# Performance work log

Measured on AMD Instinct MI355X. Metric: run time of the kernel, lower is better.

The kernel has to match this reference:

```python
import jax, jax.numpy as jnp
import numpy as np

# Gemma-style paged attention, decode-heavy continuous batching
B = 16            # number of sequences in the batch
BLOCK = 64        # KV-cache block size (tokens per block)
MAX_BLOCKS = 32   # max blocks per sequence -> max 2048 KV tokens
NUM_BLOCKS = B * MAX_BLOCKS  # 512 total cache blocks
MAX_KV = MAX_BLOCKS * BLOCK  # 2048
HQ, HK, D = 16, 8, 256       # query heads, kv heads (GQA), head_dim
HIDDEN = 3072
MAX_Q = 4                    # max new (query) tokens per sequence
ROPE_BASE = 10000.0


def setup_inputs() -> dict:
    key = jax.random.key(0)
    ks = jax.random.split(key, 7)
    # deterministic ragged layout
    q_seqlens = np.array([1 + (i % 4) for i in range(B)], np.int64)        # sum = 40
    kv_seqlens = np.array([1024 + (i * 67) % 1025 for i in range(B)], np.int64)
    q_start_loc = np.concatenate([[0], np.cumsum(q_seqlens)[:-1]]).astype(np.int64)
    T = int(q_seqlens.sum())
    history = kv_seqlens - q_seqlens
    position_ids_1d = np.concatenate(
        [np.arange(history[i], kv_seqlens[i]) for i in range(B)]).astype(np.int64)
    block_offsets = np.arange(NUM_BLOCKS, dtype=np.int64).reshape(B, MAX_BLOCKS)
    inv_freq = (1.0 / ROPE_BASE ** (np.arange(0, D, 2) / D)).astype(np.float32)
    return {
        'hidden_states': jax.random.normal(ks[0], (T, HIDDEN), jnp.float32),
        'Wq': jax.random.normal(ks[1], (HIDDEN, HQ * D), jnp.float32) * 0.02,
        'Wk': jax.random.normal(ks[2], (HIDDEN, HK * D), jnp.float32) * 0.02,
        'Wv': jax.random.normal(ks[3], (HIDDEN, HK * D), jnp.float32) * 0.02,
        'Wo': jax.random.normal(ks[4], (HQ * D, HIDDEN), jnp.float32) * 0.02,
        'k_cache': jax.random.normal(ks[5], (NUM_BLOCKS, BLOCK, HK, D), jnp.float32),
        'v_cache': jax.random.normal(ks[6], (NUM_BLOCKS, BLOCK, HK, D), jnp.float32),
        'inv_freq': jnp.asarray(inv_freq),
        'position_ids_1d': jnp.asarray(position_ids_1d),
        'q_start_loc': jnp.asarray(q_start_loc),
        'q_seqlens': jnp.asarray(q_seqlens),
        'kv_seqlens': jnp.asarray(kv_seqlens),
        'block_offsets': jnp.asarray(block_offsets),
    }


def reference(hidden_states, Wq, Wk, Wv, Wo, k_cache, v_cache, inv_freq,
              position_ids_1d, q_start_loc, q_seqlens, kv_seqlens, block_offsets):
    T = hidden_states.shape[0]
    # fused QKV projection
    q = (hidden_states @ Wq).reshape(T, HQ, D)
    k = (hidden_states @ Wk).reshape(T, HK, D)
    v = (hidden_states @ Wv).reshape(T, HK, D)
    # fused rotary embedding (neox / rotate-half style, per-token position ids)
    freqs = position_ids_1d.astype(jnp.float32)[:, None] * inv_freq[None, :]  # [T, D/2]
    cos = jnp.cos(freqs)[:, None, :]
    sin = jnp.sin(freqs)[:, None, :]

    def rope(x):
        x1, x2 = jnp.split(x, 2, axis=-1)
        return jnp.concatenate([x1 * cos - x2 * sin, x2 * cos + x1 * sin], axis=-1)

    q = rope(q)
    k = rope(k)
    # ---- fill_kv_cache: scatter new K/V into paged block cache ----
    tok = jnp.arange(T)
    seq_end = jnp.cumsum(q_seqlens)
    seq_id = jnp.searchsorted(seq_end, tok, side='right')      # sequence of each token
    off = tok - q_start_loc[seq_id]                             # offset within new tokens
    kv_pos = (kv_seqlens - q_seqlens)[seq_id] + off             # absolute kv position
    blk = block_offsets[seq_id, kv_pos // BLOCK]
    slot = kv_pos % BLOCK
    k_cache = k_cache.at[blk, slot].set(k)
    v_cache = v_cache.at[blk, slot].set(v)
    # ---- paged_attention_fwd ----
    # gather each sequence's blocks -> [B, MAX_KV, HK, D]
    k_seq = k_cache[block_offsets].reshape(B, MAX_KV, HK, D)
    v_seq = v_cache[block_offsets].reshape(B, MAX_KV, HK, D)
    # pad queries per sequence -> [B, MAX_Q, HK, G, D]
    qidx = jnp.clip(q_start_loc[:, None] + jnp.arange(MAX_Q)[None, :], 0, T - 1)
    G = HQ // HK
    qpad = q[qidx].reshape(B, MAX_Q, HK, G, D)
    scale = jnp.float32(D) ** -0.5
    scores = jnp.einsum('bqkgd,bskd->bkgqs', qpad * scale, k_seq)  # [B,HK,G,MAX_Q,MAX_KV]
    # causal mask over absolute kv positions (also masks padded kv slots)
    jpos = jnp.arange(MAX_Q)[None, :, None]
    spos = jnp.arange(MAX_KV)[None, None, :]
    mask = spos <= ((kv_seqlens - q_seqlens)[:, None, None] + jpos)  # [B,MAX_Q,MAX_KV]
    scores = jnp.where(mask[:, None, None, :, :], scores, jnp.float32(-1e30))
    attn = jax.nn.softmax(scores, axis=-1)
    out = jnp.einsum('bkgqs,bskd->bqkgd', attn, v_seq).reshape(B, MAX_Q, HQ * D)
    # scatter padded output back to flat token layout
    out_flat = out[seq_id, off]  # [T, HQ*D]
    return out_flat @ Wo
```

## Files before the change

kernel.cpp:

```cpp
#include <hip/hip_runtime.h>
#include <math.h>

#define TT 40
#define NB 16
#define HQn 16
#define HKn 8
#define Gn 2
#define Dn 256
#define HID 3072
#define QKV_COLS 8192
#define NCHUNK 16
#define CHUNKT 128

__global__ __launch_bounds__(256) void k1_qkv_gemm(
    const float* __restrict__ hs, const float* __restrict__ Wq,
    const float* __restrict__ Wk, const float* __restrict__ Wv,
    float* __restrict__ part1) {
  const int tile = blockIdx.x & 31;
  const int ks = blockIdx.x >> 5;
  const int c0 = tile << 8;
  const float* W; int ld, cw0;
  if (tile < 16)      { W = Wq; ld = 4096; cw0 = c0; }
  else if (tile < 24) { W = Wk; ld = 2048; cw0 = c0 - 4096; }
  else                { W = Wv; ld = 2048; cw0 = c0 - 6144; }
  const int kbase = ks * 192;
  const int cq = (threadIdx.x & 63) << 2;
  const int r0 = (threadIdx.x >> 6) * 10;
  __shared__ float h_lds[40][64];
  float acc[10][4];
#pragma unroll
  for (int r = 0; r < 10; ++r) { acc[r][0]=0.f; acc[r][1]=0.f; acc[r][2]=0.f; acc[r][3]=0.f; }
  for (int kc = 0; kc < 192; kc += 64) {
    __syncthreads();
    for (int i = threadIdx.x; i < 2560; i += 256) {
      int t = i >> 6, kk = i & 63;
      h_lds[t][kk] = hs[t * HID + kbase + kc + kk];
    }
    __syncthreads();
    const float* wp = W + (size_t)(kbase + kc) * ld + cw0 + cq;
#pragma unroll 8
    for (int kk = 0; kk < 64; ++kk) {
      float4 w4 = *reinterpret_cast<const float4*>(wp + (size_t)kk * ld);
#pragma unroll
      for (int r = 0; r < 10; ++r) {
        float h = h_lds[r0 + r][kk];
        acc[r][0] = fmaf(h, w4.x, acc[r][0]);
        acc[r][1] = fmaf(h, w4.y, acc[r][1]);
        acc[r][2] = fmaf(h, w4.z, acc[r][2]);
        acc[r][3] = fmaf(h, w4.w, acc[r][3]);
      }
    }
  }
#pragma unroll
  for (int r = 0; r < 10; ++r) {
    int t = r0 + r;
    float4 v = make_float4(acc[r][0], acc[r][1], acc[r][2], acc[r][3]);
    *reinterpret_cast<float4*>(&part1[(size_t)(ks * TT + t) * QKV_COLS + c0 + cq]) = v;
  }
}

__global__ __launch_bounds__(256) void k2_reduce_rope(
    const float* __restrict__ part1, const float* __restrict__ inv_freq,
    const int* __restrict__ pos_ids,
    float* __restrict__ qbuf, float* __restrict__ kbuf, float* __restrict__ vbuf) {
  const int t = blockIdx.x >> 5;
  const int tile = blockIdx.x & 31;
  const int c = (tile << 8) + threadIdx.x;
  float s = 0.f;
#pragma unroll
  for (int ks = 0; ks < 16; ++ks) s += part1[(size_t)(ks * TT + t) * QKV_COLS + c];
  __shared__ float sl[256];
  sl[threadIdx.x] = s;
  __syncthreads();
  if (tile < 24) {
    const int d = threadIdx.x;
    const int d2 = d & 127;
    float fr = (float)pos_ids[t] * inv_freq[d2];
    float cs = cosf(fr), sn = sinf(fr);
    float v = (d < 128) ? (sl[d] * cs - sl[d + 128] * sn)
                        : (sl[d] * cs + sl[d - 128] * sn);
    if (tile < 16) qbuf[t * 4096 + (tile << 8) + d] = v * 0.0625f;
    else           kbuf[t * 2048 + ((tile - 16) << 8) + d] = v;
  } else {
    vbuf[t * 2048 + ((tile - 24) << 8) + threadIdx.x] = s;
  }
}

__global__ __launch_bounds__(256) void k3_attn_partial(
    const float* __restrict__ qbuf, const float* __restrict__ kbuf,
    const float* __restrict__ vbuf, const float* __restrict__ k_cache,
    const float* __restrict__ v_cache, const int* __restrict__ blk_off,
    const int* __restrict__ q_start, const int* __restrict__ q_lens,
    const int* __restrict__ kv_lens,
    float* __restrict__ part_o, float* __restrict__ part_ml) {
  const int chunk = blockIdx.x & 15;
  const int hk = (blockIdx.x >> 4) & 7;
  const int b = blockIdx.x >> 7;
  const int kv_len = kv_lens[b];
  const int cs0 = chunk * CHUNKT;
  if (cs0 >= kv_len) return;
  const int q_cnt = q_lens[b];
  const int hist = kv_len - q_cnt;
  const int q0 = q_start[b];
  const int nq = q_cnt * 2;

  __shared__ float q_lds[8][256];
  __shared__ float S2[2][128][8];
  __shared__ float red[32][8];
  __shared__ float Mg[8];
  __shared__ float obuf[4][8][256];

  const int tid = threadIdx.x;
  const int w = tid >> 6;
  const int lane = tid & 63;
  const int tp = lane & 7;
  const int qd = lane >> 3;

  const int bi = (b << 5) + (cs0 >> 6);
  const int blk0v = blk_off[bi];
  const int blk1v = blk_off[bi + 1];
  const float* kb0  = k_cache + ((size_t)blk0v << 17) + ((size_t)hk << 8);
  const float* kb1  = k_cache + ((size_t)blk1v << 17) + ((size_t)hk << 8);
  const float* vb0  = v_cache + ((size_t)blk0v << 17) + ((size_t)hk << 8);
  const float* vb1  = v_cache + ((size_t)blk1v << 17) + ((size_t)hk << 8);
  const float* knew = kbuf + ((size_t)q0 << 11) + ((size_t)hk << 8);
  const float* vnew = vbuf + ((size_t)q0 << 11) + ((size_t)hk << 8);

  auto rowK = [&](int s) -> const float* {
    if (s < hist) {
      const float* base = (s & 64) ? kb1 : kb0;
      return base + ((size_t)(s & 63) << 11);
    }
    return knew + ((size_t)(s - hist) << 11);
  };
  auto rowV = [&](int s) -> const float* {
    if (s < hist) {
      const float* base = (s & 64) ? vb1 : vb0;
      return base + ((size_t)(s & 63) << 11);
    }
    return vnew + ((size_t)(s - hist) << 11);
  };

  for (int i = tid; i < 2048; i += 256) {
    int qv = i >> 8, d = i & 255;
    int qtok = min(qv >> 1, q_cnt - 1);
    q_lds[qv][d] = qbuf[(size_t)(q0 + qtok) * 4096 + (hk * Gn + (qv & 1)) * 256 + d];
  }
  __syncthreads();

  const int sBeg = cs0 + (w << 5);

  const float* kr[4];
#pragma unroll
  for (int tt = 0; tt < 4; ++tt) {
    int s = sBeg + (tp << 2) + tt;
    int sc = s < kv_len ? s : kv_len - 1;
    kr[tt] = rowK(sc) + (qd << 2);
  }
  float acc[4][8];
#pragma unroll
  for (int tt = 0; tt < 4; ++tt)
#pragma unroll
    for (int qv = 0; qv < 8; ++qv) acc[tt][qv] = 0.f;

#pragma unroll
  for (int c = 0; c < 8; ++c) {
    float4 kf[4];
#pragma unroll
    for (int tt = 0; tt < 4; ++tt)
      kf[tt] = *reinterpret_cast<const float4*>(kr[tt] + (c << 5));
#pragma unroll
    for (int qv = 0; qv < 8; ++qv) {
      float4 qf = *reinterpret_cast<const float4*>(&q_lds[qv][(qd << 2) + (c << 5)]);
#pragma unroll
      for (int tt = 0; tt < 4; ++tt) {
        acc[tt][qv] = fmaf(qf.x, kf[tt].x, acc[tt][qv]);
        acc[tt][qv] = fmaf(qf.y, kf[tt].y, acc[tt][qv]);
        acc[tt][qv] = fmaf(qf.z, kf[tt].z, acc[tt][qv]);
        acc[tt][qv] = fmaf(qf.w, kf[tt].w, acc[tt][qv]);
      }
    }
  }
#pragma unroll
  for (int tt = 0; tt < 4; ++tt)
#pragma unroll
    for (int qv = 0; qv < 8; ++qv) {
      float v = acc[tt][qv];
      v += __shfl_xor(v, 8);
      v += __shfl_xor(v, 16);
      acc[tt][qv] = v;
    }
  if ((lane & 24) == 0) {
    const int h = lane >> 5;
#pragma unroll
    for (int tt = 0; tt < 4; ++tt) {
      int srel = (w << 5) + (tp << 2) + tt;
      *reinterpret_cast<float4*>(&S2[h][srel][0]) =
          make_float4(acc[tt][0], acc[tt][1], acc[tt][2], acc[tt][3]);
      *reinterpret_cast<float4*>(&S2[h][srel][4]) =
          make_float4(acc[tt][4], acc[tt][5], acc[tt][6], acc[tt][7]);
    }
  }
  __syncthreads();

  const int qv2 = tid & 7;
  const int grp = tid >> 3;
  float sv[4];
  {
    float mloc = -1e30f;
#pragma unroll
    for (int t = 0; t < 4; ++t) {
      int sl = (grp << 2) + t;
      float v = S2[0][sl][qv2] + S2[1][sl][qv2];
      bool valid = (qv2 < nq) && ((cs0 + sl - hist) <= (qv2 >> 1));
      v = valid ? v : -1e30f;
      sv[t] = v;
      mloc = fmaxf(mloc, v);
    }
    red[grp][qv2] = mloc;
  }
  __syncthreads();
  if (tid < 8) {
    float M = -1e30f;
#pragma unroll
    for (int i = 0; i < 32; ++i) M = fmaxf(M, red[i][tid]);
    Mg[tid] = M;
  }
  __syncthreads();
  {
    float M = Mg[qv2];
    float lloc = 0.f;
#pragma unroll
    for (int t = 0; t < 4; ++t) {
      float p = __expf(sv[t] - M);
      S2[0][(grp << 2) + t][qv2] = p;
      lloc += p;
    }
    red[grp][qv2] = lloc;
  }
  __syncthreads();
  if (tid < 8) {
    float L = 0.f;
#pragma unroll
    for (int i = 0; i < 32; ++i) L += red[i][tid];
    int pidx = (((b * HKn + hk) * NCHUNK + chunk) << 3) + tid;
    part_ml[pidx * 2] = Mg[tid];
    part_ml[pidx * 2 + 1] = L;
  }

  float4 pacc[8];
#pragma unroll
  for (int q = 0; q < 8; ++q) pacc[q] = make_float4(0.f, 0.f, 0.f, 0.f);
  const int d4 = lane << 2;
#pragma unroll 4
  for (int t = 0; t < 32; ++t) {
    int s = sBeg + t;
    int sc = s < kv_len ? s : kv_len - 1;
    float4 vf = *reinterpret_cast<const float4*>(rowV(sc) + d4);
    int srel = (w << 5) + t;
    float4 p0 = *reinterpret_cast<const float4*>(&S2[0][srel][0]);
    float4 p1 = *reinterpret_cast<const float4*>(&S2[0][srel][4]);
    float pr[8] = {p0.x, p0.y, p0.z, p0.w, p1.x, p1.y, p1.z, p1.w};
#pragma unroll
    for (int q = 0; q < 8; ++q) {
      pacc[q].x = fmaf(pr[q], vf.x, pacc[q].x);
      pacc[q].y = fmaf(pr[q], vf.y, pacc[q].y);
      pacc[q].z = fmaf(pr[q], vf.z, pacc[q].z);
      pacc[q].w = fmaf(pr[q], vf.w, pacc[q].w);
    }
  }
#pragma unroll
  for (int q = 0; q < 8; ++q)
    *reinterpret_cast<float4*>(&obuf[w][q][d4]) = pacc[q];
  __syncthreads();

  for (int q = 0; q < nq; ++q) {
    float o = obuf[0][q][tid] + obuf[1][q][tid] + obuf[2][q][tid] + obuf[3][q][tid];
    int pidx = (((b * HKn + hk) * NCHUNK + chunk) << 3) + q;
    part_o[(size_t)pidx * 256 + tid] = o;
  }
}

__global__ __launch_bounds__(64) void k4_attn_reduce(
    const float* __restrict__ part_o, const float* __restrict__ part_ml,
    const int* __restrict__ q_start, const int* __restrict__ q_lens,
    const int* __restrict__ kv_lens, float* __restrict__ attn_out) {
  const int h = blockIdx.x & 15;
  const int qtok = (blockIdx.x >> 4) & 3;
  const int b = blockIdx.x >> 6;
  const int q_cnt = q_lens[b];
  if (qtok >= q_cnt) return;
  const int kv_len = kv_lens[b];
  const int nparts = (kv_len + CHUNKT - 1) >> 7;
  const int qv = qtok * 2 + (h & 1);
  const int hk = h >> 1;
  const int lane = threadIdx.x;
  const int pbase = ((b * HKn + hk) * NCHUNK) << 3;
  float2 mls[16];
#pragma unroll
  for (int i = 0; i < 16; ++i)
    if (i < nparts)
      mls[i] = *reinterpret_cast<const float2*>(&part_ml[(size_t)(pbase + (i << 3) + qv) * 2]);
  float M = -1e30f;
#pragma unroll
  for (int i = 0; i < 16; ++i)
    if (i < nparts) M = fmaxf(M, mls[i].x);
  float4 o = make_float4(0.f, 0.f, 0.f, 0.f);
  float L = 0.f;
#pragma unroll
  for (int i = 0; i < 16; ++i)
    if (i < nparts) {
      float corr = __expf(mls[i].x - M);
      L += corr * mls[i].y;
      float4 pv = *reinterpret_cast<const float4*>(
          &part_o[(size_t)(pbase + (i << 3) + qv) * 256 + (lane << 2)]);
      o.x = fmaf(corr, pv.x, o.x);
      o.y = fmaf(corr, pv.y, o.y);
      o.z = fmaf(corr, pv.z, o.z);
      o.w = fmaf(corr, pv.w, o.w);
    }
  float inv = 1.0f / L;
  int tr = q_start[b] + qtok;
  float4 res = make_float4(o.x * inv, o.y * inv, o.z * inv, o.w * inv);
  *reinterpret_cast<float4*>(&attn_out[((size_t)tr * HQn + h) * 256 + (lane << 2)]) = res;
}

__global__ __launch_bounds__(256) void k5_out_gemm(
    const float* __restrict__ ain, const float* __restrict__ Wo,
    float* __restrict__ part2) {
  const int tile = blockIdx.x % 12;
  const int ks = blockIdx.x / 12;
  const int c0 = tile << 8;
  const int kbase = ks << 7;
  const int cq = (threadIdx.x & 63) << 2;
  const int r0 = (threadIdx.x >> 6) * 10;
  __shared__ float h_lds[40][64];
  float acc[10][4];
#pragma unroll
  for (int r = 0; r < 10; ++r) { acc[r][0]=0.f; acc[r][1]=0.f; acc[r][2]=0.f; acc[r][3]=0.f; }
  for (int kc = 0; kc < 128; kc += 64) {
    __syncthreads();
    for (int i = threadIdx.x; i < 2560; i += 256) {
      int t = i >> 6, kk = i & 63;
      h_lds[t][kk] = ain[(size_t)t * 4096 + kbase + kc + kk];
    }
    __syncthreads();
    const float* wp = Wo + (size_t)(kbase + kc) * 3072 + c0 + cq;
#pragma unroll 8
    for (int kk = 0; kk < 64; ++kk) {
      float4 w4 = *reinterpret_cast<const float4*>(wp + (size_t)kk * 3072);
#pragma unroll
      for (int r = 0; r < 10; ++r) {
        float h = h_lds[r0 + r][kk];
        acc[r][0] = fmaf(h, w4.x, acc[r][0]);
        acc[r][1] = fmaf(h, w4.y, acc[r][1]);
        acc[r][2] = fmaf(h, w4.z, acc[r][2]);
        acc[r][3] = fmaf(h, w4.w, acc[r][3]);
      }
    }
  }
#pragma unroll
  for (int r = 0; r < 10; ++r) {
    int t = r0 + r;
    float4 v = make_float4(acc[r][0], acc[r][1], acc[r][2], acc[r][3]);
    *reinterpret_cast<float4*>(&part2[(size_t)(ks * TT + t) * 3072 + c0 + cq]) = v;
  }
}

__global__ __launch_bounds__(256) void k6_final_reduce(
    const float* __restrict__ part2, float* __restrict__ out) {
  const int idx = blockIdx.x * 256 + threadIdx.x;
  float s = 0.f;
#pragma unroll
  for (int ks = 0; ks < 32; ++ks) s += part2[(size_t)ks * 122880 + idx];
  out[idx] = s;
}

extern "C" void kernel_launch(void* const* d_in, const int* in_sizes, int n_in,
                              void* d_out, int out_size, void* d_ws, size_t ws_size,
                              hipStream_t stream) {
  const float* hs       = (const float*)d_in[0];
  const float* Wq       = (const float*)d_in[1];
  const float* Wk       = (const float*)d_in[2];
  const float* Wv       = (const float*)d_in[3];
  const float* Wo       = (const float*)d_in[4];
  const float* k_cache  = (const float*)d_in[5];
  const float* v_cache  = (const float*)d_in[6];
  const float* inv_freq = (const float*)d_in[7];
  const int*   pos_ids  = (const int*)d_in[8];
  const int*   q_start  = (const int*)d_in[9];
  const int*   q_lens   = (const int*)d_in[10];
  const int*   kv_lens  = (const int*)d_in[11];
  const int*   blk_off  = (const int*)d_in[12];

  float* ws = (float*)d_ws;
  float* qbuf     = ws;
  float* kbuf     = ws + 163840;
  float* vbuf     = ws + 245760;
  float* attn_out = ws + 327680;
  float* big      = ws + 491520;
  float* part1    = big;
  float* part_o   = big;
  float* part_ml  = big + 4194304;
  float* part2    = big;
  float* out      = (float*)d_out;

  k1_qkv_gemm<<<512, 256, 0, stream>>>(hs, Wq, Wk, Wv, part1);
  k2_reduce_rope<<<1280, 256, 0, stream>>>(part1, inv_freq, pos_ids, qbuf, kbuf, vbuf);
  k3_attn_partial<<<2048, 256, 0, stream>>>(qbuf, kbuf, vbuf, k_cache, v_cache,
                                            blk_off, q_start, q_lens, kv_lens,
                                            part_o, part_ml);
  k4_attn_reduce<<<1024, 64, 0, stream>>>(part_o, part_ml, q_start, q_lens,
                                          kv_lens, attn_out);
  k5_out_gemm<<<384, 256, 0, stream>>>(attn_out, Wo, part2);
  k6_final_reduce<<<480, 256, 0, stream>>>(part2, out);
}
```

Baseline: 290.6 us.

## Retile GEMM register blocking and restructure PV loop per query pair per wave

Both GEMM kernels switch from a 10x4 to a 5x8 register tile per thread. Hidden-state values are now read from LDS as float4 and each weight row as two float4 loads, and launch bounds ask for higher occupancy. In the attention partial kernel, each wave now owns two query vectors over the whole chunk instead of all eight over a quarter of it. This removes the obuf LDS buffer, its cross-wave reduction and a barrier, and the PV loop splits into cache-block and new-token ranges so it skips padded positions. The cost is that each wave now reads the full chunk of V rows, four times the V traffic per block, which leans on cache hits.

```diff
diff --git a/kernel.cpp b/kernel.cpp
--- a/kernel.cpp
+++ b/kernel.cpp
@@ -12,7 +12,7 @@
 #define NCHUNK 16
 #define CHUNKT 128
 
-__global__ __launch_bounds__(256) void k1_qkv_gemm(
+__global__ __launch_bounds__(256, 4) void k1_qkv_gemm(
     const float* __restrict__ hs, const float* __restrict__ Wq,
     const float* __restrict__ Wk, const float* __restrict__ Wv,
     float* __restrict__ part1) {
@@ -24,12 +24,14 @@
   else if (tile < 24) { W = Wk; ld = 2048; cw0 = c0 - 4096; }
   else                { W = Wv; ld = 2048; cw0 = c0 - 6144; }
   const int kbase = ks * 192;
-  const int cq = (threadIdx.x & 63) << 2;
-  const int r0 = (threadIdx.x >> 6) * 10;
+  const int cq = (threadIdx.x & 31) << 3;
+  const int r0 = (threadIdx.x >> 5) * 5;
   __shared__ float h_lds[40][64];
-  float acc[10][4];
-#pragma unroll
-  for (int r = 0; r < 10; ++r) { acc[r][0]=0.f; acc[r][1]=0.f; acc[r][2]=0.f; acc[r][3]=0.f; }
+  float acc[5][8];
+#pragma unroll
+  for (int r = 0; r < 5; ++r)
+#pragma unroll
+    for (int c = 0; c < 8; ++c) acc[r][c] = 0.f;
   for (int kc = 0; kc < 192; kc += 64) {
     __syncthreads();
     for (int i = threadIdx.x; i < 2560; i += 256) {
@@ -38,24 +40,38 @@
     }
     __syncthreads();
     const float* wp = W + (size_t)(kbase + kc) * ld + cw0 + cq;
-#pragma unroll 8
-    for (int kk = 0; kk < 64; ++kk) {
-      float4 w4 = *reinterpret_cast<const float4*>(wp + (size_t)kk * ld);
-#pragma unroll
-      for (int r = 0; r < 10; ++r) {
-        float h = h_lds[r0 + r][kk];
-        acc[r][0] = fmaf(h, w4.x, acc[r][0]);
-        acc[r][1] = fmaf(h, w4.y, acc[r][1]);
-        acc[r][2] = fmaf(h, w4.z, acc[r][2]);
-        acc[r][3] = fmaf(h, w4.w, acc[r][3]);
+#pragma unroll 2
+    for (int k4 = 0; k4 < 16; ++k4) {
+      float4 h4[5];
+#pragma unroll
+      for (int r = 0; r < 5; ++r)
+        h4[r] = *reinterpret_cast<const float4*>(&h_lds[r0 + r][k4 << 2]);
+#pragma unroll
+      for (int j = 0; j < 4; ++j) {
+        const float* wr = wp + (size_t)((k4 << 2) + j) * ld;
+        float4 wa = *reinterpret_cast<const float4*>(wr);
+        float4 wb = *reinterpret_cast<const float4*>(wr + 4);
+#pragma unroll
+        for (int r = 0; r < 5; ++r) {
+          float hv = (j == 0) ? h4[r].x : (j == 1) ? h4[r].y : (j == 2) ? h4[r].z : h4[r].w;
+          acc[r][0] = fmaf(hv, wa.x, acc[r][0]);
+          acc[r][1] = fmaf(hv, wa.y, acc[r][1]);
+          acc[r][2] = fmaf(hv, wa.z, acc[r][2]);
+          acc[r][3] = fmaf(hv, wa.w, acc[r][3]);
+          acc[r][4] = fmaf(hv, wb.x, acc[r][4]);
+          acc[r][5] = fmaf(hv, wb.y, acc[r][5]);
+          acc[r][6] = fmaf(hv, wb.z, acc[r][6]);
+          acc[r][7] = fmaf(hv, wb.w, acc[r][7]);
+        }
       }
     }
   }
 #pragma unroll
-  for (int r = 0; r < 10; ++r) {
+  for (int r = 0; r < 5; ++r) {
     int t = r0 + r;
-    float4 v = make_float4(acc[r][0], acc[r][1], acc[r][2], acc[r][3]);
-    *reinterpret_cast<float4*>(&part1[(size_t)(ks * TT + t) * QKV_COLS + c0 + cq]) = v;
+    float* dst = &part1[(size_t)(ks * TT + t) * QKV_COLS + c0 + cq];
+    *reinterpret_cast<float4*>(dst) = make_float4(acc[r][0], acc[r][1], acc[r][2], acc[r][3]);
+    *reinterpret_cast<float4*>(dst + 4) = make_float4(acc[r][4], acc[r][5], acc[r][6], acc[r][7]);
   }
 }
 
@@ -86,7 +102,7 @@
   }
 }
 
-__global__ __launch_bounds__(256) void k3_attn_partial(
+__global__ __launch_bounds__(256, 6) void k3_attn_partial(
     const float* __restrict__ qbuf, const float* __restrict__ kbuf,
     const float* __restrict__ vbuf, const float* __restrict__ k_cache,
     const float* __restrict__ v_cache, const int* __restrict__ blk_off,
@@ -108,7 +124,6 @@
   __shared__ float S2[2][128][8];
   __shared__ float red[32][8];
   __shared__ float Mg[8];
-  __shared__ float obuf[4][8][256];
 
   const int tid = threadIdx.x;
   const int w = tid >> 6;
@@ -133,13 +148,6 @@
     }
     return knew + ((size_t)(s - hist) << 11);
   };
-  auto rowV = [&](int s) -> const float* {
-    if (s < hist) {
-      const float* base = (s & 64) ? vb1 : vb0;
-      return base + ((size_t)(s & 63) << 11);
-    }
-    return vnew + ((size_t)(s - hist) << 11);
-  };
 
   for (int i = tid; i < 2048; i += 256) {
     int qv = i >> 8, d = i & 255;
@@ -248,36 +256,42 @@
     part_ml[pidx * 2 + 1] = L;
   }
 
-  float4 pacc[8];
-#pragma unroll
-  for (int q = 0; q < 8; ++q) pacc[q] = make_float4(0.f, 0.f, 0.f, 0.f);
+  const int qp = w << 1;
   const int d4 = lane << 2;
+  float4 a0 = make_float4(0.f, 0.f, 0.f, 0.f);
+  float4 a1 = make_float4(0.f, 0.f, 0.f, 0.f);
+  const int lim = min(cs0 + CHUNKT, kv_len);
+
+#define PV_STEP(VROW, SREL)                                          \
+  {                                                                  \
+    float4 vf = *reinterpret_cast<const float4*>(VROW);              \
+    float2 pp = *reinterpret_cast<const float2*>(&S2[0][SREL][qp]);  \
+    a0.x = fmaf(pp.x, vf.x, a0.x); a0.y = fmaf(pp.x, vf.y, a0.y);    \
+    a0.z = fmaf(pp.x, vf.z, a0.z); a0.w = fmaf(pp.x, vf.w, a0.w);    \
+    a1.x = fmaf(pp.y, vf.x, a1.x); a1.y = fmaf(pp.y, vf.y, a1.y);    \
+    a1.z = fmaf(pp.y, vf.z, a1.z); a1.w = fmaf(pp.y, vf.w, a1.w);    \
+  }
+
+  {
+    int eA = min(min(cs0 + 64, hist), lim);
 #pragma unroll 4
-  for (int t = 0; t < 32; ++t) {
-    int s = sBeg + t;
-    int sc = s < kv_len ? s : kv_len - 1;
-    float4 vf = *reinterpret_cast<const float4*>(rowV(sc) + d4);
-    int srel = (w << 5) + t;
-    float4 p0 = *reinterpret_cast<const float4*>(&S2[0][srel][0]);
-    float4 p1 = *reinterpret_cast<const float4*>(&S2[0][srel][4]);
-    float pr[8] = {p0.x, p0.y, p0.z, p0.w, p1.x, p1.y, p1.z, p1.w};
-#pragma unroll
-    for (int q = 0; q < 8; ++q) {
-      pacc[q].x = fmaf(pr[q], vf.x, pacc[q].x);
-      pacc[q].y = fmaf(pr[q], vf.y, pacc[q].y);
-      pacc[q].z = fmaf(pr[q], vf.z, pacc[q].z);
-      pacc[q].w = fmaf(pr[q], vf.w, pacc[q].w);
-    }
-  }
-#pragma unroll
-  for (int q = 0; q < 8; ++q)
-    *reinterpret_cast<float4*>(&obuf[w][q][d4]) = pacc[q];
-  __syncthreads();
-
-  for (int q = 0; q < nq; ++q) {
-    float o = obuf[0][q][tid] + obuf[1][q][tid] + obuf[2][q][tid] + obuf[3][q][tid];
-    int pidx = (((b * HKn + hk) * NCHUNK + chunk) << 3) + q;
-    part_o[(size_t)pidx * 256 + tid] = o;
+    for (int s = cs0; s < eA; ++s)
+      PV_STEP(vb0 + ((size_t)(s & 63) << 11) + d4, s - cs0);
+    int eB = min(min(cs0 + 128, hist), lim);
+#pragma unroll 4
+    for (int s = cs0 + 64; s < eB; ++s)
+      PV_STEP(vb1 + ((size_t)(s & 63) << 11) + d4, s - cs0);
+    int bC = max(cs0, hist);
+#pragma unroll
+    for (int s = bC; s < lim; ++s)
+      PV_STEP(vnew + ((size_t)(s - hist) << 11) + d4, s - cs0);
+  }
+#undef PV_STEP
+
+  if (qp < nq) {
+    int pidxb = (((b * HKn + hk) * NCHUNK + chunk) << 3) + qp;
+    *reinterpret_cast<float4*>(&part_o[(size_t)pidxb * 256 + d4]) = a0;
+    *reinterpret_cast<float4*>(&part_o[(size_t)(pidxb + 1) * 256 + d4]) = a1;
   }
 }
 
@@ -325,19 +339,21 @@
   *reinterpret_cast<float4*>(&attn_out[((size_t)tr * HQn + h) * 256 + (lane << 2)]) = res;
 }
 
-__global__ __launch_bounds__(256) void k5_out_gemm(
+__global__ __launch_bounds__(256, 4) void k5_out_gemm(
     const float* __restrict__ ain, const float* __restrict__ Wo,
     float* __restrict__ part2) {
   const int tile = blockIdx.x % 12;
   const int ks = blockIdx.x / 12;
   const int c0 = tile << 8;
   const int kbase = ks << 7;
-  const int cq = (threadIdx.x & 63) << 2;
-  const int r0 = (threadIdx.x >> 6) * 10;
+  const int cq = (threadIdx.x & 31) << 3;
+  const int r0 = (threadIdx.x >> 5) * 5;
   __shared__ float h_lds[40][64];
-  float acc[10][4];
-#pragma unroll
-  for (int r = 0; r < 10; ++r) { acc[r][0]=0.f; acc[r][1]=0.f; acc[r][2]=0.f; acc[r][3]=0.f; }
+  float acc[5][8];
+#pragma unroll
+  for (int r = 0; r < 5; ++r)
+#pragma unroll
+    for (int c = 0; c < 8; ++c) acc[r][c] = 0.f;
   for (int kc = 0; kc < 128; kc += 64) {
     __syncthreads();
     for (int i = threadIdx.x; i < 2560; i += 256) {
@@ -346,24 +362,38 @@
     }
     __syncthreads();
     const float* wp = Wo + (size_t)(kbase + kc) * 3072 + c0 + cq;
-#pragma unroll 8
-    for (int kk = 0; kk < 64; ++kk) {
-      float4 w4 = *reinterpret_cast<const float4*>(wp + (size_t)kk * 3072);
-#pragma unroll
-      for (int r = 0; r < 10; ++r) {
-        float h = h_lds[r0 + r][kk];
-        acc[r][0] = fmaf(h, w4.x, acc[r][0]);
-        acc[r][1] = fmaf(h, w4.y, acc[r][1]);
-        acc[r][2] = fmaf(h, w4.z, acc[r][2]);
-        acc[r][3] = fmaf(h, w4.w, acc[r][3]);
+#pragma unroll 2
+    for (int k4 = 0; k4 < 16; ++k4) {
+      float4 h4[5];
+#pragma unroll
+      for (int r = 0; r < 5; ++r)
+        h4[r] = *reinterpret_cast<const float4*>(&h_lds[r0 + r][k4 << 2]);
+#pragma unroll
+      for (int j = 0; j < 4; ++j) {
+        const float* wr = wp + (size_t)((k4 << 2) + j) * 3072;
+        float4 wa = *reinterpret_cast<const float4*>(wr);
+        float4 wb = *reinterpret_cast<const float4*>(wr + 4);
+#pragma unroll
+        for (int r = 0; r < 5; ++r) {
+          float hv = (j == 0) ? h4[r].x : (j == 1) ? h4[r].y : (j == 2) ? h4[r].z : h4[r].w;
+          acc[r][0] = fmaf(hv, wa.x, acc[r][0]);
+          acc[r][1] = fmaf(hv, wa.y, acc[r][1]);
+          acc[r][2] = fmaf(hv, wa.z, acc[r][2]);
+          acc[r][3] = fmaf(hv, wa.w, acc[r][3]);
+          acc[r][4] = fmaf(hv, wb.x, acc[r][4]);
+          acc[r][5] = fmaf(hv, wb.y, acc[r][5]);
+          acc[r][6] = fmaf(hv, wb.z, acc[r][6]);
+          acc[r][7] = fmaf(hv, wb.w, acc[r][7]);
+        }
       }
     }
   }
 #pragma unroll
-  for (int r = 0; r < 10; ++r) {
+  for (int r = 0; r < 5; ++r) {
     int t = r0 + r;
-    float4 v = make_float4(acc[r][0], acc[r][1], acc[r][2], acc[r][3]);
-    *reinterpret_cast<float4*>(&part2[(size_t)(ks * TT + t) * 3072 + c0 + cq]) = v;
+    float* dst = &part2[(size_t)(ks * TT + t) * 3072 + c0 + cq];
+    *reinterpret_cast<float4*>(dst) = make_float4(acc[r][0], acc[r][1], acc[r][2], acc[r][3]);
+    *reinterpret_cast<float4*>(dst + 4) = make_float4(acc[r][4], acc[r][5], acc[r][6], acc[r][7]);
   }
 }
 
```

Result: slower. 365.5 us (+25.8%).

## Split Q and KV projections; overlap KV GEMM with history attention

Applied to the files above, without the earlier changes.

The QKV GEMM is split so only the Q projection runs before attention. The K/V projection GEMM is packed into the same launch as the attention pass over cached history tokens, so the two can overlap. The new tokens' K/V are folded into the last history partial by a small follow-up kernel that does an online-softmax merge. The P·V stage is also reorganised so each wave handles two query vectors across all 128 tokens, which removes the shared-memory obuf reduction and lowers LDS use. This adds two launches, and it assumes every sequence has history > 0 and that new tokens land in the last chunk slot.

```diff
diff --git a/kernel.cpp b/kernel.cpp
--- a/kernel.cpp
+++ b/kernel.cpp
@@ -2,27 +2,18 @@
 #include <math.h>
 
 #define TT 40
-#define NB 16
-#define HQn 16
 #define HKn 8
 #define Gn 2
-#define Dn 256
 #define HID 3072
-#define QKV_COLS 8192
 #define NCHUNK 16
 #define CHUNKT 128
 
-__global__ __launch_bounds__(256) void k1_qkv_gemm(
+__global__ __launch_bounds__(256) void k1q(
     const float* __restrict__ hs, const float* __restrict__ Wq,
-    const float* __restrict__ Wk, const float* __restrict__ Wv,
-    float* __restrict__ part1) {
-  const int tile = blockIdx.x & 31;
-  const int ks = blockIdx.x >> 5;
+    float* __restrict__ part1q) {
+  const int tile = blockIdx.x & 15;
+  const int ks = blockIdx.x >> 4;
   const int c0 = tile << 8;
-  const float* W; int ld, cw0;
-  if (tile < 16)      { W = Wq; ld = 4096; cw0 = c0; }
-  else if (tile < 24) { W = Wk; ld = 2048; cw0 = c0 - 4096; }
-  else                { W = Wv; ld = 2048; cw0 = c0 - 6144; }
   const int kbase = ks * 192;
   const int cq = (threadIdx.x & 63) << 2;
   const int r0 = (threadIdx.x >> 6) * 10;
@@ -37,10 +28,10 @@
       h_lds[t][kk] = hs[t * HID + kbase + kc + kk];
     }
     __syncthreads();
-    const float* wp = W + (size_t)(kbase + kc) * ld + cw0 + cq;
+    const float* wp = Wq + (size_t)(kbase + kc) * 4096 + c0 + cq;
 #pragma unroll 8
     for (int kk = 0; kk < 64; ++kk) {
-      float4 w4 = *reinterpret_cast<const float4*>(wp + (size_t)kk * ld);
+      float4 w4 = *reinterpret_cast<const float4*>(wp + (size_t)kk * 4096);
 #pragma unroll
       for (int r = 0; r < 10; ++r) {
         float h = h_lds[r0 + r][kk];
@@ -55,62 +46,99 @@
   for (int r = 0; r < 10; ++r) {
     int t = r0 + r;
     float4 v = make_float4(acc[r][0], acc[r][1], acc[r][2], acc[r][3]);
-    *reinterpret_cast<float4*>(&part1[(size_t)(ks * TT + t) * QKV_COLS + c0 + cq]) = v;
-  }
-}
-
-__global__ __launch_bounds__(256) void k2_reduce_rope(
-    const float* __restrict__ part1, const float* __restrict__ inv_freq,
-    const int* __restrict__ pos_ids,
-    float* __restrict__ qbuf, float* __restrict__ kbuf, float* __restrict__ vbuf) {
-  const int t = blockIdx.x >> 5;
-  const int tile = blockIdx.x & 31;
+    *reinterpret_cast<float4*>(&part1q[(size_t)(ks * TT + t) * 4096 + c0 + cq]) = v;
+  }
+}
+
+__global__ __launch_bounds__(256) void k2q(
+    const float* __restrict__ part1q, const float* __restrict__ inv_freq,
+    const int* __restrict__ pos_ids, float* __restrict__ qbuf) {
+  const int t = blockIdx.x >> 4;
+  const int tile = blockIdx.x & 15;
   const int c = (tile << 8) + threadIdx.x;
   float s = 0.f;
 #pragma unroll
-  for (int ks = 0; ks < 16; ++ks) s += part1[(size_t)(ks * TT + t) * QKV_COLS + c];
+  for (int ks = 0; ks < 16; ++ks) s += part1q[(size_t)(ks * TT + t) * 4096 + c];
   __shared__ float sl[256];
   sl[threadIdx.x] = s;
   __syncthreads();
-  if (tile < 24) {
-    const int d = threadIdx.x;
-    const int d2 = d & 127;
-    float fr = (float)pos_ids[t] * inv_freq[d2];
-    float cs = cosf(fr), sn = sinf(fr);
-    float v = (d < 128) ? (sl[d] * cs - sl[d + 128] * sn)
-                        : (sl[d] * cs + sl[d - 128] * sn);
-    if (tile < 16) qbuf[t * 4096 + (tile << 8) + d] = v * 0.0625f;
-    else           kbuf[t * 2048 + ((tile - 16) << 8) + d] = v;
-  } else {
-    vbuf[t * 2048 + ((tile - 24) << 8) + threadIdx.x] = s;
-  }
-}
-
-__global__ __launch_bounds__(256) void k3_attn_partial(
-    const float* __restrict__ qbuf, const float* __restrict__ kbuf,
-    const float* __restrict__ vbuf, const float* __restrict__ k_cache,
+  const int d = threadIdx.x;
+  float fr = (float)pos_ids[t] * inv_freq[d & 127];
+  float cs = cosf(fr), sn = sinf(fr);
+  float v = (d < 128) ? (sl[d] * cs - sl[d + 128] * sn)
+                      : (sl[d] * cs + sl[d - 128] * sn);
+  qbuf[t * 4096 + (tile << 8) + d] = v * 0.0625f;
+}
+
+__global__ __launch_bounds__(256) void kA(
+    const float* __restrict__ hs, const float* __restrict__ Wk,
+    const float* __restrict__ Wv, float* __restrict__ part1kv,
+    const float* __restrict__ qbuf, const float* __restrict__ k_cache,
     const float* __restrict__ v_cache, const int* __restrict__ blk_off,
     const int* __restrict__ q_start, const int* __restrict__ q_lens,
     const int* __restrict__ kv_lens,
     float* __restrict__ part_o, float* __restrict__ part_ml) {
-  const int chunk = blockIdx.x & 15;
-  const int hk = (blockIdx.x >> 4) & 7;
-  const int b = blockIdx.x >> 7;
-  const int kv_len = kv_lens[b];
+  __shared__ __align__(16) char smem[17440];
+  const int tid = threadIdx.x;
+
+  if (blockIdx.x < 96) {
+    const int tile = blockIdx.x & 15;
+    const int ks = blockIdx.x >> 4;
+    const float* W = (tile < 8) ? Wk : Wv;
+    const int cw0 = (tile & 7) << 8;
+    const int kbase = ks << 9;
+    const int cq = (tid & 63) << 2;
+    const int r0 = (tid >> 6) * 10;
+    float (*h_lds)[64] = (float (*)[64])smem;
+    float acc[10][4];
+#pragma unroll
+    for (int r = 0; r < 10; ++r) { acc[r][0]=0.f; acc[r][1]=0.f; acc[r][2]=0.f; acc[r][3]=0.f; }
+    for (int kc = 0; kc < 512; kc += 64) {
+      __syncthreads();
+      for (int i = tid; i < 2560; i += 256) {
+        int t = i >> 6, kk = i & 63;
+        h_lds[t][kk] = hs[t * HID + kbase + kc + kk];
+      }
+      __syncthreads();
+      const float* wp = W + (size_t)(kbase + kc) * 2048 + cw0 + cq;
+#pragma unroll 8
+      for (int kk = 0; kk < 64; ++kk) {
+        float4 w4 = *reinterpret_cast<const float4*>(wp + (size_t)kk * 2048);
+#pragma unroll
+        for (int r = 0; r < 10; ++r) {
+          float h = h_lds[r0 + r][kk];
+          acc[r][0] = fmaf(h, w4.x, acc[r][0]);
+          acc[r][1] = fmaf(h, w4.y, acc[r][1]);
+          acc[r][2] = fmaf(h, w4.z, acc[r][2]);
+          acc[r][3] = fmaf(h, w4.w, acc[r][3]);
+        }
+      }
+    }
+#pragma unroll
+    for (int r = 0; r < 10; ++r) {
+      int t = r0 + r;
+      float4 v = make_float4(acc[r][0], acc[r][1], acc[r][2], acc[r][3]);
+      *reinterpret_cast<float4*>(&part1kv[(size_t)(ks * TT + t) * 4096 + (tile << 8) + cq]) = v;
+    }
+    return;
+  }
+
+  const int v = blockIdx.x - 96;
+  const int chunk = v & 15;
+  const int hk = (v >> 4) & 7;
+  const int b = v >> 7;
+  const int q_cnt = q_lens[b];
+  const int hist = kv_lens[b] - q_cnt;
   const int cs0 = chunk * CHUNKT;
-  if (cs0 >= kv_len) return;
-  const int q_cnt = q_lens[b];
-  const int hist = kv_len - q_cnt;
+  if (cs0 >= hist) return;
   const int q0 = q_start[b];
   const int nq = q_cnt * 2;
 
-  __shared__ float q_lds[8][256];
-  __shared__ float S2[2][128][8];
-  __shared__ float red[32][8];
-  __shared__ float Mg[8];
-  __shared__ float obuf[4][8][256];
-
-  const int tid = threadIdx.x;
+  float (*q_lds)[256] = (float (*)[256])smem;
+  float (*S2)[128][8] = (float (*)[128][8])(smem + 8192);
+  float (*red)[8]     = (float (*)[8])(smem + 16384);
+  float* Mg           = (float*)(smem + 17408);
+
   const int w = tid >> 6;
   const int lane = tid & 63;
   const int tp = lane & 7;
@@ -119,27 +147,10 @@
   const int bi = (b << 5) + (cs0 >> 6);
   const int blk0v = blk_off[bi];
   const int blk1v = blk_off[bi + 1];
-  const float* kb0  = k_cache + ((size_t)blk0v << 17) + ((size_t)hk << 8);
-  const float* kb1  = k_cache + ((size_t)blk1v << 17) + ((size_t)hk << 8);
-  const float* vb0  = v_cache + ((size_t)blk0v << 17) + ((size_t)hk << 8);
-  const float* vb1  = v_cache + ((size_t)blk1v << 17) + ((size_t)hk << 8);
-  const float* knew = kbuf + ((size_t)q0 << 11) + ((size_t)hk << 8);
-  const float* vnew = vbuf + ((size_t)q0 << 11) + ((size_t)hk << 8);
-
-  auto rowK = [&](int s) -> const float* {
-    if (s < hist) {
-      const float* base = (s & 64) ? kb1 : kb0;
-      return base + ((size_t)(s & 63) << 11);
-    }
-    return knew + ((size_t)(s - hist) << 11);
-  };
-  auto rowV = [&](int s) -> const float* {
-    if (s < hist) {
-      const float* base = (s & 64) ? vb1 : vb0;
-      return base + ((size_t)(s & 63) << 11);
-    }
-    return vnew + ((size_t)(s - hist) << 11);
-  };
+  const float* kb0 = k_cache + ((size_t)blk0v << 17) + ((size_t)hk << 8);
+  const float* kb1 = k_cache + ((size_t)blk1v << 17) + ((size_t)hk << 8);
+  const float* vb0 = v_cache + ((size_t)blk0v << 17) + ((size_t)hk << 8);
+  const float* vb1 = v_cache + ((size_t)blk1v << 17) + ((size_t)hk << 8);
 
   for (int i = tid; i < 2048; i += 256) {
     int qv = i >> 8, d = i & 255;
@@ -154,15 +165,14 @@
 #pragma unroll
   for (int tt = 0; tt < 4; ++tt) {
     int s = sBeg + (tp << 2) + tt;
-    int sc = s < kv_len ? s : kv_len - 1;
-    kr[tt] = rowK(sc) + (qd << 2);
+    int sc = s < hist ? s : hist - 1;
+    kr[tt] = (((sc & 64) ? kb1 : kb0) + ((size_t)(sc & 63) << 11)) + (qd << 2);
   }
   float acc[4][8];
 #pragma unroll
   for (int tt = 0; tt < 4; ++tt)
 #pragma unroll
     for (int qv = 0; qv < 8; ++qv) acc[tt][qv] = 0.f;
-
 #pragma unroll
   for (int c = 0; c < 8; ++c) {
     float4 kf[4];
@@ -185,10 +195,10 @@
   for (int tt = 0; tt < 4; ++tt)
 #pragma unroll
     for (int qv = 0; qv < 8; ++qv) {
-      float v = acc[tt][qv];
-      v += __shfl_xor(v, 8);
-      v += __shfl_xor(v, 16);
-      acc[tt][qv] = v;
+      float val = acc[tt][qv];
+      val += __shfl_xor(val, 8);
+      val += __shfl_xor(val, 16);
+      acc[tt][qv] = val;
     }
   if ((lane & 24) == 0) {
     const int h = lane >> 5;
@@ -211,11 +221,10 @@
 #pragma unroll
     for (int t = 0; t < 4; ++t) {
       int sl = (grp << 2) + t;
-      float v = S2[0][sl][qv2] + S2[1][sl][qv2];
-      bool valid = (qv2 < nq) && ((cs0 + sl - hist) <= (qv2 >> 1));
-      v = valid ? v : -1e30f;
-      sv[t] = v;
-      mloc = fmaxf(mloc, v);
+      float val = S2[0][sl][qv2] + S2[1][sl][qv2];
+      val = (cs0 + sl < hist) ? val : -1e30f;
+      sv[t] = val;
+      mloc = fmaxf(mloc, val);
     }
     red[grp][qv2] = mloc;
   }
@@ -247,37 +256,133 @@
     part_ml[pidx * 2] = Mg[tid];
     part_ml[pidx * 2 + 1] = L;
   }
-
-  float4 pacc[8];
-#pragma unroll
-  for (int q = 0; q < 8; ++q) pacc[q] = make_float4(0.f, 0.f, 0.f, 0.f);
+  __syncthreads();
+
+  const int qp = w << 1;
   const int d4 = lane << 2;
+  float4 a0 = make_float4(0.f, 0.f, 0.f, 0.f);
+  float4 a1 = make_float4(0.f, 0.f, 0.f, 0.f);
 #pragma unroll 4
-  for (int t = 0; t < 32; ++t) {
-    int s = sBeg + t;
-    int sc = s < kv_len ? s : kv_len - 1;
-    float4 vf = *reinterpret_cast<const float4*>(rowV(sc) + d4);
-    int srel = (w << 5) + t;
-    float4 p0 = *reinterpret_cast<const float4*>(&S2[0][srel][0]);
-    float4 p1 = *reinterpret_cast<const float4*>(&S2[0][srel][4]);
-    float pr[8] = {p0.x, p0.y, p0.z, p0.w, p1.x, p1.y, p1.z, p1.w};
-#pragma unroll
-    for (int q = 0; q < 8; ++q) {
-      pacc[q].x = fmaf(pr[q], vf.x, pacc[q].x);
-      pacc[q].y = fmaf(pr[q], vf.y, pacc[q].y);
-      pacc[q].z = fmaf(pr[q], vf.z, pacc[q].z);
-      pacc[q].w = fmaf(pr[q], vf.w, pacc[q].w);
-    }
-  }
-#pragma unroll
-  for (int q = 0; q < 8; ++q)
-    *reinterpret_cast<float4*>(&obuf[w][q][d4]) = pacc[q];
-  __syncthreads();
-
-  for (int q = 0; q < nq; ++q) {
-    float o = obuf[0][q][tid] + obuf[1][q][tid] + obuf[2][q][tid] + obuf[3][q][tid];
-    int pidx = (((b * HKn + hk) * NCHUNK + chunk) << 3) + q;
-    part_o[(size_t)pidx * 256 + tid] = o;
+  for (int s2 = 0; s2 < 128; ++s2) {
+    int sc = cs0 + s2;
+    sc = sc < hist ? sc : hist - 1;
+    const float* vrow = ((sc & 64) ? vb1 : vb0) + ((size_t)(sc & 63) << 11);
+    float4 vf = *reinterpret_cast<const float4*>(vrow + d4);
+    float2 pp = *reinterpret_cast<const float2*>(&S2[0][s2][qp]);
+    a0.x = fmaf(pp.x, vf.x, a0.x); a0.y = fmaf(pp.x, vf.y, a0.y);
+    a0.z = fmaf(pp.x, vf.z, a0.z); a0.w = fmaf(pp.x, vf.w, a0.w);
+    a1.x = fmaf(pp.y, vf.x, a1.x); a1.y = fmaf(pp.y, vf.y, a1.y);
+    a1.z = fmaf(pp.y, vf.z, a1.z); a1.w = fmaf(pp.y, vf.w, a1.w);
+  }
+  int pidxb = (((b * HKn + hk) * NCHUNK + chunk) << 3) + qp;
+  *reinterpret_cast<float4*>(&part_o[(size_t)pidxb * 256 + d4]) = a0;
+  *reinterpret_cast<float4*>(&part_o[(size_t)(pidxb + 1) * 256 + d4]) = a1;
+}
+
+__global__ __launch_bounds__(256) void k2kv(
+    const float* __restrict__ part1kv, const float* __restrict__ inv_freq,
+    const int* __restrict__ pos_ids,
+    float* __restrict__ kbuf, float* __restrict__ vbuf) {
+  const int t = blockIdx.x >> 4;
+  const int tile = blockIdx.x & 15;
+  const int c = (tile << 8) + threadIdx.x;
+  float s = 0.f;
+#pragma unroll
+  for (int ks = 0; ks < 6; ++ks) s += part1kv[(size_t)(ks * TT + t) * 4096 + c];
+  __shared__ float sl[256];
+  sl[threadIdx.x] = s;
+  __syncthreads();
+  if (tile < 8) {
+    const int d = threadIdx.x;
+    float fr = (float)pos_ids[t] * inv_freq[d & 127];
+    float cs = cosf(fr), sn = sinf(fr);
+    float v = (d < 128) ? (sl[d] * cs - sl[d + 128] * sn)
+                        : (sl[d] * cs + sl[d - 128] * sn);
+    kbuf[t * 2048 + (tile << 8) + d] = v;
+  } else {
+    vbuf[t * 2048 + ((tile - 8) << 8) + threadIdx.x] = s;
+  }
+}
+
+__global__ __launch_bounds__(256) void k3new(
+    const float* __restrict__ qbuf, const float* __restrict__ kbuf,
+    const float* __restrict__ vbuf, const int* __restrict__ q_start,
+    const int* __restrict__ q_lens, const int* __restrict__ kv_lens,
+    float* __restrict__ part_o, float* __restrict__ part_ml) {
+  const int hk = blockIdx.x & 7;
+  const int b = blockIdx.x >> 3;
+  const int q_cnt = q_lens[b];
+  const int hist = kv_lens[b] - q_cnt;
+  const int q0 = q_start[b];
+  const int nq = q_cnt * 2;
+  const int npH = (hist + 127) >> 7;
+  const int slot = npH - 1;
+
+  __shared__ float S[4][8];
+  __shared__ float pf[4][8];
+  __shared__ float e1s[8];
+
+  const int tid = threadIdx.x;
+  const int w = tid >> 6;
+  const int lane = tid & 63;
+
+  if (w < q_cnt) {
+    const int qv = lane & 7;
+    const int dg = lane >> 3;
+    const float* kp = kbuf + (size_t)(q0 + w) * 2048 + (hk << 8) + (dg << 5);
+    const float* qp = qbuf + (size_t)(q0 + min(qv >> 1, q_cnt - 1)) * 4096
+                    + (hk * Gn + (qv & 1)) * 256 + (dg << 5);
+    float sc = 0.f;
+#pragma unroll
+    for (int j = 0; j < 8; ++j) {
+      float4 kf = *reinterpret_cast<const float4*>(kp + (j << 2));
+      float4 qf = *reinterpret_cast<const float4*>(qp + (j << 2));
+      sc = fmaf(qf.x, kf.x, sc); sc = fmaf(qf.y, kf.y, sc);
+      sc = fmaf(qf.z, kf.z, sc); sc = fmaf(qf.w, kf.w, sc);
+    }
+    sc += __shfl_xor(sc, 8);
+    sc += __shfl_xor(sc, 16);
+    sc += __shfl_xor(sc, 32);
+    if (lane < 8) {
+      bool valid = (lane < nq) && (w <= (lane >> 1));
+      S[w][lane] = valid ? sc : -1e30f;
+    }
+  }
+  __syncthreads();
+
+  if (tid < 8) {
+    if (tid < nq) {
+      int pidx = (((b * HKn + hk) * NCHUNK + slot) << 3) + tid;
+      float M1 = part_ml[pidx * 2];
+      float L1 = part_ml[pidx * 2 + 1];
+      float m2 = -1e30f;
+      for (int j = 0; j < q_cnt; ++j) m2 = fmaxf(m2, S[j][tid]);
+      float M = fmaxf(M1, m2);
+      float e1 = __expf(M1 - M);
+      float l2 = 0.f;
+      for (int j = 0; j < q_cnt; ++j) {
+        float p = __expf(S[j][tid] - M);
+        pf[j][tid] = p;
+        l2 += p;
+      }
+      e1s[tid] = e1;
+      part_ml[pidx * 2] = M;
+      part_ml[pidx * 2 + 1] = e1 * L1 + l2;
+    } else {
+      e1s[tid] = 0.f;
+    }
+  }
+  __syncthreads();
+
+  for (int i = tid; i < 2048; i += 256) {
+    int qv = i >> 8, d = i & 255;
+    if (qv < nq) {
+      size_t oidx = (size_t)((((b * HKn + hk) * NCHUNK + slot) << 3) + qv) * 256 + d;
+      float acc = e1s[qv] * part_o[oidx];
+      for (int j = 0; j < q_cnt; ++j)
+        acc = fmaf(pf[j][qv], vbuf[(size_t)(q0 + j) * 2048 + (hk << 8) + d], acc);
+      part_o[oidx] = acc;
+    }
   }
 }
 
@@ -290,8 +395,8 @@
   const int b = blockIdx.x >> 6;
   const int q_cnt = q_lens[b];
   if (qtok >= q_cnt) return;
-  const int kv_len = kv_lens[b];
-  const int nparts = (kv_len + CHUNKT - 1) >> 7;
+  const int hist = kv_lens[b] - q_cnt;
+  const int nparts = (hist + 127) >> 7;
   const int qv = qtok * 2 + (h & 1);
   const int hk = h >> 1;
   const int lane = threadIdx.x;
@@ -322,7 +427,7 @@
   float inv = 1.0f / L;
   int tr = q_start[b] + qtok;
   float4 res = make_float4(o.x * inv, o.y * inv, o.z * inv, o.w * inv);
-  *reinterpret_cast<float4*>(&attn_out[((size_t)tr * HQn + h) * 256 + (lane << 2)]) = res;
+  *reinterpret_cast<float4*>(&attn_out[((size_t)tr * 16 + h) * 256 + (lane << 2)]) = res;
 }
 
 __global__ __launch_bounds__(256) void k5_out_gemm(
@@ -399,17 +504,20 @@
   float* vbuf     = ws + 245760;
   float* attn_out = ws + 327680;
   float* big      = ws + 491520;
-  float* part1    = big;
+  float* part1q   = big;
   float* part_o   = big;
   float* part_ml  = big + 4194304;
+  float* part1kv  = big + 4227072;
   float* part2    = big;
   float* out      = (float*)d_out;
 
-  k1_qkv_gemm<<<512, 256, 0, stream>>>(hs, Wq, Wk, Wv, part1);
-  k2_reduce_rope<<<1280, 256, 0, stream>>>(part1, inv_freq, pos_ids, qbuf, kbuf, vbuf);
-  k3_attn_partial<<<2048, 256, 0, stream>>>(qbuf, kbuf, vbuf, k_cache, v_cache,
-                                            blk_off, q_start, q_lens, kv_lens,
-                                            part_o, part_ml);
+  k1q <<<256, 256, 0, stream>>>(hs, Wq, part1q);
+  k2q <<<640, 256, 0, stream>>>(part1q, inv_freq, pos_ids, qbuf);
+  kA  <<<2144, 256, 0, stream>>>(hs, Wk, Wv, part1kv, qbuf, k_cache, v_cache,
+                                 blk_off, q_start, q_lens, kv_lens, part_o, part_ml);
+  k2kv<<<640, 256, 0, stream>>>(part1kv, inv_freq, pos_ids, kbuf, vbuf);
+  k3new<<<128, 256, 0, stream>>>(qbuf, kbuf, vbuf, q_start, q_lens, kv_lens,
+                                 part_o, part_ml);
   k4_attn_reduce<<<1024, 64, 0, stream>>>(part_o, part_ml, q_start, q_lens,
                                           kv_lens, attn_out);
   k5_out_gemm<<<384, 256, 0, stream>>>(attn_out, Wo, part2);
```

After: 374.5 us. 1.29x slower.

## Split PV accumulation by query pair per wave, drop LDS cross-wave reduction

Applied to the files above, without the earlier changes.

The P·V stage changes its work split. Before, each of the 4 waves covered 32 KV rows for all 8 query vectors and the partial outputs were summed through a 32KB LDS buffer and a barrier. Now each wave owns two query vectors and walks every valid KV row in the chunk, splitting the loop by block segment so no per-row branch or clamp is needed. This removes the obuf LDS traffic, the barrier and the padded-row work, and cuts accumulator registers from 32 to 8. In exchange every wave now reads all V rows for the chunk, so global/L2 V reads per block rise about fourfold.

```diff
diff --git a/kernel.cpp b/kernel.cpp
--- a/kernel.cpp
+++ b/kernel.cpp
@@ -108,7 +108,6 @@
   __shared__ float S2[2][128][8];
   __shared__ float red[32][8];
   __shared__ float Mg[8];
-  __shared__ float obuf[4][8][256];
 
   const int tid = threadIdx.x;
   const int w = tid >> 6;
@@ -133,13 +132,6 @@
     }
     return knew + ((size_t)(s - hist) << 11);
   };
-  auto rowV = [&](int s) -> const float* {
-    if (s < hist) {
-      const float* base = (s & 64) ? vb1 : vb0;
-      return base + ((size_t)(s & 63) << 11);
-    }
-    return vnew + ((size_t)(s - hist) << 11);
-  };
 
   for (int i = tid; i < 2048; i += 256) {
     int qv = i >> 8, d = i & 255;
@@ -248,36 +240,42 @@
     part_ml[pidx * 2 + 1] = L;
   }
 
-  float4 pacc[8];
-#pragma unroll
-  for (int q = 0; q < 8; ++q) pacc[q] = make_float4(0.f, 0.f, 0.f, 0.f);
+  const int qp = w << 1;
   const int d4 = lane << 2;
+  float4 a0 = make_float4(0.f, 0.f, 0.f, 0.f);
+  float4 a1 = make_float4(0.f, 0.f, 0.f, 0.f);
+  const int lim = min(cs0 + CHUNKT, kv_len);
+
+#define PV_STEP(VROW, SREL)                                          \
+  {                                                                  \
+    float4 vf = *reinterpret_cast<const float4*>(VROW);              \
+    float2 pp = *reinterpret_cast<const float2*>(&S2[0][SREL][qp]);  \
+    a0.x = fmaf(pp.x, vf.x, a0.x); a0.y = fmaf(pp.x, vf.y, a0.y);    \
+    a0.z = fmaf(pp.x, vf.z, a0.z); a0.w = fmaf(pp.x, vf.w, a0.w);    \
+    a1.x = fmaf(pp.y, vf.x, a1.x); a1.y = fmaf(pp.y, vf.y, a1.y);    \
+    a1.z = fmaf(pp.y, vf.z, a1.z); a1.w = fmaf(pp.y, vf.w, a1.w);    \
+  }
+
+  {
+    int eA = min(min(cs0 + 64, hist), lim);
 #pragma unroll 4
-  for (int t = 0; t < 32; ++t) {
-    int s = sBeg + t;
-    int sc = s < kv_len ? s : kv_len - 1;
-    float4 vf = *reinterpret_cast<const float4*>(rowV(sc) + d4);
-    int srel = (w << 5) + t;
-    float4 p0 = *reinterpret_cast<const float4*>(&S2[0][srel][0]);
-    float4 p1 = *reinterpret_cast<const float4*>(&S2[0][srel][4]);
-    float pr[8] = {p0.x, p0.y, p0.z, p0.w, p1.x, p1.y, p1.z, p1.w};
-#pragma unroll
-    for (int q = 0; q < 8; ++q) {
-      pacc[q].x = fmaf(pr[q], vf.x, pacc[q].x);
-      pacc[q].y = fmaf(pr[q], vf.y, pacc[q].y);
-      pacc[q].z = fmaf(pr[q], vf.z, pacc[q].z);
-      pacc[q].w = fmaf(pr[q], vf.w, pacc[q].w);
-    }
-  }
-#pragma unroll
-  for (int q = 0; q < 8; ++q)
-    *reinterpret_cast<float4*>(&obuf[w][q][d4]) = pacc[q];
-  __syncthreads();
-
-  for (int q = 0; q < nq; ++q) {
-    float o = obuf[0][q][tid] + obuf[1][q][tid] + obuf[2][q][tid] + obuf[3][q][tid];
-    int pidx = (((b * HKn + hk) * NCHUNK + chunk) << 3) + q;
-    part_o[(size_t)pidx * 256 + tid] = o;
+    for (int s = cs0; s < eA; ++s)
+      PV_STEP(vb0 + ((size_t)(s & 63) << 11) + d4, s - cs0);
+    int eB = min(min(cs0 + 128, hist), lim);
+#pragma unroll 4
+    for (int s = cs0 + 64; s < eB; ++s)
+      PV_STEP(vb1 + ((size_t)(s & 63) << 11) + d4, s - cs0);
+    int bC = max(cs0, hist);
+#pragma unroll
+    for (int s = bC; s < lim; ++s)
+      PV_STEP(vnew + ((size_t)(s - hist) << 11) + d4, s - cs0);
+  }
+#undef PV_STEP
+
+  if (qp < nq) {
+    int pidxb = (((b * HKn + hk) * NCHUNK + chunk) << 3) + qp;
+    *reinterpret_cast<float4*>(&part_o[(size_t)pidxb * 256 + d4]) = a0;
+    *reinterpret_cast<float4*>(&part_o[(size_t)(pidxb + 1) * 256 + d4]) = a1;
   }
 }
 
```

Measured after the change: 308.8 us. 6.3% more time.
